# Performance work log

Measured on AMD Instinct MI355X. Metric: run time of the kernel, lower is better.

Reference implementation:

```python
import jax, jax.numpy as jnp
import numpy as np
import math

H, W = 512, 1024
PS = 2
H_p, W_p = H // PS, W // PS
N = 9
C_IN, C_OUT = 128, 64
GROUPS = 32
B = 2
EPS_GN = 1e-5


def _make_grid():
    # Replicates LatDeform2xDown buffers: centers + sec(lat)-scaled 3x3 offsets.
    pr = np.arange(H_p, dtype=np.float32) * PS + (PS - 1) / 2
    pc = np.arange(W_p, dtype=np.float32) * PS + (PS - 1) / 2
    cy = pr / (H - 1) * 2 - 1
    cx = pc / (W - 1) * 2 - 1
    centers = np.stack([np.broadcast_to(cx[None, :], (H_p, W_p)),
                        np.broadcast_to(cy[:, None], (H_p, W_p))], axis=-1)  # (H_p,W_p,2)
    delta = math.pi / (H - 1)  # drop_south_pole = False
    lat = math.pi / 2 - pr * delta
    sec_max = W / 4.0
    sec = np.clip(1.0 / np.cos(lat), -sec_max, sec_max).astype(np.float32)
    ky, kx = np.meshgrid(np.array([-1.0, 0.0, 1.0], np.float32),
                         np.array([-1.0, 0.0, 1.0], np.float32), indexing='ij')
    kxf, kyf = kx.flatten(), ky.flatten()
    dx = (kxf[None, :] * sec[:, None]) / (W - 1) * 2          # (H_p, 9)
    dy = np.broadcast_to(kyf[None, :], (H_p, N)) / (H - 1) * 2  # (H_p, 9)
    offsets = np.stack([dx, dy], axis=-1)                      # (H_p, 9, 2)
    locs = centers[:, :, None, :] + offsets[:, None, :, :]     # (H_p, W_p, 9, 2)
    return jnp.asarray(locs.reshape(-1, 2).astype(np.float32))


def group_norm(x, gamma, beta, groups, eps=EPS_GN):
    b, c, h, w = x.shape
    xg = x.reshape(b, groups, c // groups, h, w)
    mu = xg.mean(axis=(2, 3, 4), keepdims=True)
    var = ((xg - mu) ** 2).mean(axis=(2, 3, 4), keepdims=True)
    xn = ((xg - mu) * jax.lax.rsqrt(var + eps)).reshape(b, c, h, w)
    return xn * gamma[None, :, None, None] + beta[None, :, None, None]


def setup_inputs() -> dict:
    key = jax.random.key(0)
    ks = jax.random.split(key, 3)
    x = jax.random.normal(ks[0], (B, C_IN, H_p, W_p), dtype=jnp.float32)
    w_conv = jax.random.normal(ks[1], (N * C_OUT, C_IN), dtype=jnp.float32) * 0.02
    w_post = jax.random.normal(ks[2], (C_OUT, C_OUT), dtype=jnp.float32) * 0.05
    return {
        'x': x,
        'grid': _make_grid(),
        'gamma1': jnp.ones((C_IN,), jnp.float32),
        'beta1': jnp.zeros((C_IN,), jnp.float32),
        'w_conv': w_conv,
        'splat_bias': jnp.zeros((C_OUT,), jnp.float32),
        'w_post': w_post,
        'b_post': jnp.zeros((C_OUT,), jnp.float32),
        'gamma2': jnp.ones((C_OUT,), jnp.float32),
        'beta2': jnp.zeros((C_OUT,), jnp.float32),
    }


def reference(x, grid, gamma1, beta1, w_conv, splat_bias, w_post, b_post, gamma2, beta2):
    b = x.shape[0]
    # norm + 1x1 conv (no bias): Wx part of the Wx+b split
    h = group_norm(x, gamma1, beta1, GROUPS)
    vals = jnp.einsum('oc,bchw->bohw', w_conv, h)                 # (B, 9*C, H_p, W_p)
    vals = vals.reshape(b, C_OUT, N, H_p, W_p).transpose(0, 1, 3, 4, 2)
    vals = vals.reshape(b, C_OUT, H_p * W_p * N)                  # (B, C, M)

    # bilinear splat coordinates
    px = (grid[:, 0] + 1.0) * 0.5 * (W - 1)                       # (M,)
    py = (grid[:, 1] + 1.0) * 0.5 * (H - 1)
    x0 = jnp.floor(px).astype(jnp.int32)
    y0 = jnp.floor(py).astype(jnp.int32)
    x1, y1 = x0 + 1, y0 + 1
    fx = px - x0.astype(px.dtype)
    fy = py - y0.astype(py.dtype)
    w00 = (1 - fx) * (1 - fy)
    w01 = (1 - fx) * fy
    w10 = fx * (1 - fy)
    w11 = fx * fy
    x0w = x0 % W
    x1w = x1 % W
    half_W = W // 2

    def polar_wrap(yi, xi):
        past_n = yi < 0
        past_s = yi >= H
        yi = jnp.where(past_n, -yi, yi)
        yi = jnp.where(past_s, 2 * H - yi, yi)
        xi = jnp.where(past_n | past_s, (xi + half_W) % W, xi)
        return jnp.clip(yi, 0, H - 1), xi

    num = jnp.zeros((b, C_OUT, H * W), x.dtype)
    den = jnp.zeros((H * W,), x.dtype)  # identical across batch in the original
    for wt, yi, xi in ((w00, y0, x0w), (w01, y1, x0w), (w10, y0, x1w), (w11, y1, x1w)):
        yi, xi = polar_wrap(yi, xi)
        idx = yi * W + xi                                          # (M,)
        num = num.at[:, :, idx].add(vals * wt[None, None, :])
        den = den.at[idx].add(wt)

    out = num / jnp.clip(den, 1e-8)[None, None, :]
    out = out.reshape(b, C_OUT, H, W) + splat_bias[None, :, None, None]
    # post: 1x1 conv + GroupNorm + exact GELU
    out = jnp.einsum('oc,bchw->bohw', w_post, out) + b_post[None, :, None, None]
    out = group_norm(out, gamma2, beta2, GROUPS)
    return jax.nn.gelu(out, approximate=False)
```

## Files before the change

kernel.cpp:

```cpp
#include <hip/hip_runtime.h>
#include <cstdint>
#include <cstddef>

#define H_   512
#define W_   1024
#define HP_  256
#define WP_  512
#define NTAP 9
#define CIN  128
#define COUT 64
#define HWP  (HP_*WP_)
#define MIDX (HWP*NTAP)
#define HW_  (H_*W_)

typedef __attribute__((ext_vector_type(8))) short bhalf8_t;
typedef __attribute__((ext_vector_type(4))) float floatx4_t;

__device__ __forceinline__ unsigned short f2bf(float f) {
    unsigned u = __float_as_uint(f);
    u += 0x7fffu + ((u >> 16) & 1u);
    return (unsigned short)(u >> 16);
}
__device__ __forceinline__ float bf2f(unsigned short s) {
    return __uint_as_float(((unsigned)s) << 16);
}

__global__ __launch_bounds__(256) void k0_prep(
    const float* __restrict__ w_conv, const float* __restrict__ w_post,
    unsigned short* __restrict__ w2, unsigned short* __restrict__ wpostbf,
    float* __restrict__ gnzero ) {
    int idx = blockIdx.x * 256 + threadIdx.x;
    if (idx < 576*128) {
        int r = idx >> 7, c = idx & 127;
        int o = r / 9, n = r % 9;
        w2[((n*64 + o) << 7) + c] = f2bf(w_conv[idx]);
    } else if (idx < 576*128 + 4096) {
        int i2 = idx - 576*128;
        wpostbf[i2] = f2bf(w_post[i2]);
    } else if (idx < 576*128 + 4096 + 256) {
        gnzero[idx - (576*128 + 4096)] = 0.f;
    }
}

__global__ __launch_bounds__(256) void k1_stats(const float* __restrict__ x,
                                                float* __restrict__ gnsum1) {
    __shared__ float red[512];
    int bid = blockIdx.x;
    int b = bid >> 8, rem = bid & 255;
    int g = rem >> 3, slice = rem & 7;
    const float4* xp = (const float4*)x + (size_t)(b*CIN + g*4) * (HWP/4) + (size_t)slice*16384;
    float s = 0.f, s2 = 0.f;
    for (int i = threadIdx.x; i < 16384; i += 256) {
        float4 v = xp[i];
        s  += v.x + v.y + v.z + v.w;
        s2 += v.x*v.x + v.y*v.y + v.z*v.z + v.w*v.w;
    }
    red[threadIdx.x] = s; red[256 + threadIdx.x] = s2;
    __syncthreads();
    for (int off = 128; off > 0; off >>= 1) {
        if (threadIdx.x < off) {
            red[threadIdx.x] += red[threadIdx.x + off];
            red[256 + threadIdx.x] += red[256 + threadIdx.x + off];
        }
        __syncthreads();
    }
    if (threadIdx.x == 0) {
        atomicAdd(&gnsum1[(b*32 + g)*2],     red[0]);
        atomicAdd(&gnsum1[(b*32 + g)*2 + 1], red[256]);
    }
}

__global__ void k1b_coef(const float* __restrict__ gnsum1,
                         const float* __restrict__ gamma1, const float* __restrict__ beta1,
                         float* __restrict__ acoef, float* __restrict__ bcoef) {
    int t = threadIdx.x;
    int b = t >> 7, c = t & 127, g = c >> 2;
    float s1 = gnsum1[(b*32+g)*2], s2 = gnsum1[(b*32+g)*2+1];
    const float inv = 1.f / 524288.f;
    float mean = s1 * inv;
    float var  = s2 * inv - mean*mean;
    float rstd = rsqrtf(var + 1e-5f);
    float a = gamma1[c] * rstd;
    acoef[t] = a;
    bcoef[t] = beta1[c] - mean * a;
}

__global__ __launch_bounds__(256) void k2_conv(
    const float* __restrict__ x, const unsigned short* __restrict__ w2,
    const float* __restrict__ acoef, const float* __restrict__ bcoef,
    unsigned short* __restrict__ vals) {
    __shared__ unsigned short As[64*136];
    __shared__ unsigned short Bs[128*136];
    __shared__ unsigned short Cs[128*72];
    int b   = blockIdx.y;
    int tile = blockIdx.x;
    int pr  = tile >> 2, pcb = (tile & 3) << 7;
    int tid = threadIdx.x;

    for (int task = tid; task < 2048; task += 256) {
        int p = task & 127, c0 = (task >> 7) << 3;
        bhalf8_t t8;
        #pragma unroll
        for (int j = 0; j < 8; ++j) {
            int c = c0 + j;
            float xv = x[(size_t)(b*CIN + c)*HWP + (size_t)pr*WP_ + pcb + p];
            float v = fmaf(xv, acoef[b*CIN + c], bcoef[b*CIN + c]);
            t8[j] = (short)f2bf(v);
        }
        *(bhalf8_t*)&Bs[p*136 + c0] = t8;
    }
    __syncthreads();

    int wave = tid >> 6, lane = tid & 63;
    int l15 = lane & 15, lq = lane >> 4;

    bhalf8_t bfr[2][4];
    #pragma unroll
    for (int ptl = 0; ptl < 2; ++ptl) {
        int p = (wave*2 + ptl)*16 + l15;
        #pragma unroll
        for (int ks = 0; ks < 4; ++ks)
            bfr[ptl][ks] = *(const bhalf8_t*)&Bs[p*136 + ks*32 + lq*8];
    }

    for (int n = 0; n < 9; ++n) {
        __syncthreads();
        for (int i = tid; i < 4096; i += 256) {
            int r = i >> 6, cp = i & 63;
            ((unsigned*)As)[r*68 + cp] = ((const unsigned*)w2)[(n*64 + r)*64 + cp];
        }
        __syncthreads();
        floatx4_t acc[2][4] = {};
        #pragma unroll
        for (int ks = 0; ks < 4; ++ks) {
            bhalf8_t af[4];
            #pragma unroll
            for (int rt = 0; rt < 4; ++rt)
                af[rt] = *(const bhalf8_t*)&As[(rt*16 + l15)*136 + ks*32 + lq*8];
            #pragma unroll
            for (int ptl = 0; ptl < 2; ++ptl)
                #pragma unroll
                for (int rt = 0; rt < 4; ++rt)
                    acc[ptl][rt] = __builtin_amdgcn_mfma_f32_16x16x32_bf16(
                        af[rt], bfr[ptl][ks], acc[ptl][rt], 0, 0, 0);
        }
        #pragma unroll
        for (int ptl = 0; ptl < 2; ++ptl) {
            int p = (wave*2 + ptl)*16 + l15;
            #pragma unroll
            for (int rt = 0; rt < 4; ++rt)
                #pragma unroll
                for (int reg = 0; reg < 4; ++reg) {
                    int o = rt*16 + lq*4 + reg;
                    Cs[p*72 + o] = f2bf(acc[ptl][rt][reg]);
                }
        }
        __syncthreads();
        size_t outbase = (size_t)b*HWP + (size_t)pr*WP_ + pcb;
        for (int i = tid; i < 4096; i += 256) {
            int p = i >> 5, o2 = i & 31;
            ((unsigned*)vals)[((outbase + p)*576 + n*64)/2 + o2] = ((const unsigned*)Cs)[p*36 + o2];
        }
    }
}

__global__ __launch_bounds__(256) void k3_gather(
    const float* __restrict__ gridp, const unsigned short* __restrict__ vals,
    const unsigned short* __restrict__ wpostbf,
    const float* __restrict__ splat_bias, const float* __restrict__ b_post,
    float* __restrict__ out, float* __restrict__ gnsum2) {

    __shared__ unsigned short SM[256*72];
    __shared__ unsigned short WPs[64*72];
    __shared__ float sb_s[64], bp_s[64], gsum[64];

    int tid = threadIdx.x;
    int bx = blockIdx.x;
    int y  = blockIdx.y;
    int b  = blockIdx.z;
    int x  = (bx << 8) + tid;

    if (tid < 64) { sb_s[tid] = splat_bias[tid]; bp_s[tid] = b_post[tid]; gsum[tid] = 0.f; }
    for (int i = tid; i < 2048; i += 256) {
        int r = i >> 5, cp = i & 31;
        ((unsigned*)WPs)[r*36 + cp] = ((const unsigned*)wpostbf)[(r << 5) + cp];
    }

    float num[64];
    #pragma unroll
    for (int c = 0; c < 64; ++c) num[c] = 0.f;
    float den = 0.f;

    const float2* g2 = (const float2*)gridp;
    int prc = y >> 1;
    for (int dpr = -1; dpr <= 1; ++dpr) {
        int pr = prc + dpr;
        if (pr < 0 || pr > HP_-1) continue;
        for (int kyi = 0; kyi < 3; ++kyi) {
            float gy = g2[pr*WP_*9 + kyi*3 + 1].y;
            float py = ((gy + 1.0f) * 0.5f) * 511.0f;
            float y0f = floorf(py);
            float fy = py - y0f;
            int y0i = (int)y0f;
            #pragma unroll
            for (int side = 0; side < 2; ++side) {
                int yi = y0i + side;
                bool pn = yi < 0, ps = yi >= H_;
                int yy = pn ? -yi : (ps ? (2*H_ - yi) : yi);
                yy = min(max(yy, 0), H_-1);
                if (yy != y) continue;
                int sh = (pn || ps) ? (W_/2) : 0;
                float wy = side ? fy : (1.0f - fy);
                for (int kxi = 0; kxi < 3; ++kxi) {
                    int n = kyi*3 + kxi;
                    float gx0 = g2[pr*WP_*9 + n].x;
                    float px0 = ((gx0 + 1.0f) * 0.5f) * 1023.0f;
                    int Tt = x - sh - 1;
                    #pragma unroll
                    for (int j = -1; j <= 1; ++j) {
                        float A = ((float)(Tt + j*W_) - px0) * 0.5f;
                        int clo = (int)ceilf(A - 1e-3f);
                        int chi = (int)floorf(A + 1.001f);
                        for (int pc = clo; pc <= chi; ++pc) {
                            if (pc < 0 || pc >= WP_) continue;
                            int m = (pr*WP_ + pc)*9 + n;
                            float2 g = g2[m];
                            float px = ((g.x + 1.0f) * 0.5f) * 1023.0f;
                            float x0f = floorf(px);
                            float fx = px - x0f;
                            int x0i = (int)x0f;
                            int xl = (x0i + 2*W_ + sh) & (W_-1);
                            float w;
                            if (xl == x)                      w = (1.0f - fx) * wy;
                            else if (((xl + 1) & (W_-1)) == x) w = fx * wy;
                            else continue;
                            den += w;
                            const uint4* vp = (const uint4*)(vals + (((size_t)b*MIDX + m) << 6));
                            #pragma unroll
                            for (int q = 0; q < 8; ++q) {
                                uint4 u = vp[q];
                                unsigned uu[4] = {u.x, u.y, u.z, u.w};
                                #pragma unroll
                                for (int e = 0; e < 4; ++e) {
                                    float lo = __uint_as_float(uu[e] << 16);
                                    float hi = __uint_as_float(uu[e] & 0xffff0000u);
                                    num[q*8 + e*2]     = fmaf(w, lo, num[q*8 + e*2]);
                                    num[q*8 + e*2 + 1] = fmaf(w, hi, num[q*8 + e*2 + 1]);
                                }
                            }
                        }
                    }
                }
            }
        }
    }

    float invd = 1.0f / fmaxf(den, 1e-8f);
    {
        int base = tid * 72;
        #pragma unroll
        for (int c8 = 0; c8 < 8; ++c8) {
            bhalf8_t t8;
            #pragma unroll
            for (int jj = 0; jj < 8; ++jj) {
                float v = fmaf(num[c8*8 + jj], invd, sb_s[c8*8 + jj]);
                t8[jj] = (short)f2bf(v);
            }
            *(bhalf8_t*)&SM[base + c8*8] = t8;
        }
    }
    __syncthreads();

    int wave = tid >> 6, lane = tid & 63, l15 = lane & 15, lq = lane >> 4;
    floatx4_t acc[4][4] = {};
    #pragma unroll
    for (int ks = 0; ks < 2; ++ks) {
        bhalf8_t af[4], bf[4];
        #pragma unroll
        for (int ot = 0; ot < 4; ++ot)
            af[ot] = *(const bhalf8_t*)&WPs[(ot*16 + l15)*72 + ks*32 + lq*8];
        #pragma unroll
        for (int pt = 0; pt < 4; ++pt)
            bf[pt] = *(const bhalf8_t*)&SM[((wave*4 + pt)*16 + l15)*72 + ks*32 + lq*8];
        #pragma unroll
        for (int pt = 0; pt < 4; ++pt)
            #pragma unroll
            for (int ot = 0; ot < 4; ++ot)
                acc[pt][ot] = __builtin_amdgcn_mfma_f32_16x16x32_bf16(
                    af[ot], bf[pt], acc[pt][ot], 0, 0, 0);
    }

    float s1l[8], s2l[8];
    #pragma unroll
    for (int li = 0; li < 8; ++li) { s1l[li] = 0.f; s2l[li] = 0.f; }
    #pragma unroll
    for (int pt = 0; pt < 4; ++pt) {
        int px = (wave*4 + pt)*16 + l15;
        int xg = (bx << 8) + px;
        #pragma unroll
        for (int ot = 0; ot < 4; ++ot)
            #pragma unroll
            for (int reg = 0; reg < 4; ++reg) {
                int o = ot*16 + lq*4 + reg;
                float v = acc[pt][ot][reg] + bp_s[o];
                out[((size_t)(b*64 + o) << 19) + ((size_t)y << 10) + xg] = v;
                int li = ot*2 + (reg >> 1);
                s1l[li] += v;
                s2l[li] += v*v;
            }
    }
    #pragma unroll
    for (int li = 0; li < 8; ++li) {
        int g = (li >> 1)*8 + lq*2 + (li & 1);
        atomicAdd(&gsum[g*2],     s1l[li]);
        atomicAdd(&gsum[g*2 + 1], s2l[li]);
    }
    __syncthreads();
    if (tid < 64) atomicAdd(&gnsum2[b*64 + tid], gsum[tid]);
}

__global__ __launch_bounds__(256) void k5_final(
    float* __restrict__ out, const float* __restrict__ gnsum2,
    const float* __restrict__ gamma2, const float* __restrict__ beta2) {
    size_t idx = (size_t)blockIdx.x * 256 + threadIdx.x;
    size_t e8 = idx << 3;
    int b = (int)(e8 >> 25);
    int o = (int)((e8 >> 19) & 63);
    int g = o >> 1;
    float s1 = gnsum2[b*64 + g*2], s2 = gnsum2[b*64 + g*2 + 1];
    const float invn = 1.0f / 1048576.0f;
    float mean = s1 * invn;
    float var  = s2 * invn - mean*mean;
    float rstd = rsqrtf(var + 1e-5f);
    float sc = gamma2[o] * rstd;
    float sf = beta2[o] - mean * sc;
    float4* p0 = (float4*)(out + e8);
    float4 v0 = p0[0], v1 = p0[1];
    float r[8] = {v0.x, v0.y, v0.z, v0.w, v1.x, v1.y, v1.z, v1.w};
    #pragma unroll
    for (int j = 0; j < 8; ++j) {
        float t = fmaf(r[j], sc, sf);
        r[j] = 0.5f * t * (1.0f + erff(t * 0.70710678118654752f));
    }
    p0[0] = make_float4(r[0], r[1], r[2], r[3]);
    p0[1] = make_float4(r[4], r[5], r[6], r[7]);
}

extern "C" void kernel_launch(void* const* d_in, const int* in_sizes, int n_in,
                              void* d_out, int out_size, void* d_ws, size_t ws_size,
                              hipStream_t stream) {
    const float* x      = (const float*)d_in[0];
    const float* gridp  = (const float*)d_in[1];
    const float* gamma1 = (const float*)d_in[2];
    const float* beta1  = (const float*)d_in[3];
    const float* w_conv = (const float*)d_in[4];
    const float* sbias  = (const float*)d_in[5];
    const float* w_post = (const float*)d_in[6];
    const float* b_post = (const float*)d_in[7];
    const float* gamma2 = (const float*)d_in[8];
    const float* beta2  = (const float*)d_in[9];
    float* out = (float*)d_out;

    char* ws = (char*)d_ws;
    unsigned short* w2      = (unsigned short*)(ws);
    unsigned short* wpostbf = (unsigned short*)(ws + 147456);
    float* gnsum1 = (float*)(ws + 155648);
    float* gnsum2 = (float*)(ws + 156160);
    float* acoef  = (float*)(ws + 156672);
    float* bcoef  = (float*)(ws + 157696);
    unsigned short* vals = (unsigned short*)(ws + 158720);

    hipLaunchKernelGGL(k0_prep,  dim3(305),          dim3(256), 0, stream,
                       w_conv, w_post, w2, wpostbf, gnsum1);
    hipLaunchKernelGGL(k1_stats, dim3(512),          dim3(256), 0, stream, x, gnsum1);
    hipLaunchKernelGGL(k1b_coef, dim3(1),            dim3(256), 0, stream,
                       gnsum1, gamma1, beta1, acoef, bcoef);
    hipLaunchKernelGGL(k2_conv,  dim3(1024, 2),      dim3(256), 0, stream,
                       x, w2, acoef, bcoef, vals);
    hipLaunchKernelGGL(k3_gather, dim3(4, 512, 2),   dim3(256), 0, stream,
                       gridp, vals, wpostbf, sbias, b_post, out, gnsum2);
    hipLaunchKernelGGL(k5_final, dim3(32768),        dim3(256), 0, stream,
                       out, gnsum2, gamma2, beta2);
}
```

Baseline: 994.8 us.

## Fold post 1x1 conv weights into deform conv weights, drop MFMA stage in gather

```diff
diff --git a/kernel.cpp b/kernel.cpp
--- a/kernel.cpp
+++ b/kernel.cpp
@@ -27,18 +27,26 @@
 
 __global__ __launch_bounds__(256) void k0_prep(
     const float* __restrict__ w_conv, const float* __restrict__ w_post,
-    unsigned short* __restrict__ w2, unsigned short* __restrict__ wpostbf,
+    const float* __restrict__ sbias,  const float* __restrict__ b_post,
+    unsigned short* __restrict__ w2, float* __restrict__ sb2,
     float* __restrict__ gnzero ) {
     int idx = blockIdx.x * 256 + threadIdx.x;
-    if (idx < 576*128) {
-        int r = idx >> 7, c = idx & 127;
-        int o = r / 9, n = r % 9;
-        w2[((n*64 + o) << 7) + c] = f2bf(w_conv[idx]);
-    } else if (idx < 576*128 + 4096) {
-        int i2 = idx - 576*128;
-        wpostbf[i2] = f2bf(w_post[i2]);
-    } else if (idx < 576*128 + 4096 + 256) {
-        gnzero[idx - (576*128 + 4096)] = 0.f;
+    if (idx < 73728) {
+        int r = idx >> 7, ci = idx & 127;
+        int n = r >> 6, o = r & 63;
+        float acc = 0.f;
+        #pragma unroll 8
+        for (int op = 0; op < 64; ++op)
+            acc = fmaf(w_post[o*64 + op], w_conv[(op*9 + n)*128 + ci], acc);
+        w2[idx] = f2bf(acc);
+    } else if (idx < 73728 + 64) {
+        int o = idx - 73728;
+        float acc = b_post[o];
+        for (int op = 0; op < 64; ++op)
+            acc = fmaf(w_post[o*64 + op], sbias[op], acc);
+        sb2[o] = acc;
+    } else if (idx < 73728 + 64 + 256) {
+        gnzero[idx - (73728 + 64)] = 0.f;
     }
 }
 
@@ -166,13 +174,11 @@
 
 __global__ __launch_bounds__(256) void k3_gather(
     const float* __restrict__ gridp, const unsigned short* __restrict__ vals,
-    const unsigned short* __restrict__ wpostbf,
-    const float* __restrict__ splat_bias, const float* __restrict__ b_post,
+    const float* __restrict__ sb2g,
     float* __restrict__ out, float* __restrict__ gnsum2) {
 
-    __shared__ unsigned short SM[256*72];
-    __shared__ unsigned short WPs[64*72];
-    __shared__ float sb_s[64], bp_s[64], gsum[64];
+    __shared__ float sb2_s[64];
+    __shared__ float red[256];
 
     int tid = threadIdx.x;
     int bx = blockIdx.x;
@@ -180,11 +186,8 @@
     int b  = blockIdx.z;
     int x  = (bx << 8) + tid;
 
-    if (tid < 64) { sb_s[tid] = splat_bias[tid]; bp_s[tid] = b_post[tid]; gsum[tid] = 0.f; }
-    for (int i = tid; i < 2048; i += 256) {
-        int r = i >> 5, cp = i & 31;
-        ((unsigned*)WPs)[r*36 + cp] = ((const unsigned*)wpostbf)[(r << 5) + cp];
-    }
+    if (tid < 64) sb2_s[tid] = sb2g[tid];
+    __syncthreads();
 
     float num[64];
     #pragma unroll
@@ -256,67 +259,75 @@
     }
 
     float invd = 1.0f / fmaxf(den, 1e-8f);
-    {
-        int base = tid * 72;
-        #pragma unroll
-        for (int c8 = 0; c8 < 8; ++c8) {
-            bhalf8_t t8;
-            #pragma unroll
-            for (int jj = 0; jj < 8; ++jj) {
-                float v = fmaf(num[c8*8 + jj], invd, sb_s[c8*8 + jj]);
-                t8[jj] = (short)f2bf(v);
-            }
-            *(bhalf8_t*)&SM[base + c8*8] = t8;
-        }
-    }
+    size_t obase = ((size_t)b << 25) + ((size_t)y << 10) + (size_t)x;
+    #pragma unroll
+    for (int c = 0; c < 64; ++c) {
+        float v = fmaf(num[c], invd, sb2_s[c]);
+        out[obase + ((size_t)c << 19)] = v;
+        num[c] = v;
+    }
+
+    float st[64];
+    #pragma unroll
+    for (int g = 0; g < 32; ++g) {
+        float a = num[2*g], b2 = num[2*g + 1];
+        st[g]      = a + b2;
+        st[32 + g] = fmaf(a, a, b2*b2);
+    }
+    int lane = tid & 63;
+    float r32[32];
+    { bool hi = (lane & 32) != 0;
+      #pragma unroll
+      for (int j = 0; j < 32; ++j) {
+          float keep = hi ? st[32+j] : st[j];
+          float send = hi ? st[j]    : st[32+j];
+          r32[j] = keep + __shfl_xor(send, 32, 64);
+      } }
+    float r16[16];
+    { bool hi = (lane & 16) != 0;
+      #pragma unroll
+      for (int j = 0; j < 16; ++j) {
+          float keep = hi ? r32[16+j] : r32[j];
+          float send = hi ? r32[j]    : r32[16+j];
+          r16[j] = keep + __shfl_xor(send, 16, 64);
+      } }
+    float r8[8];
+    { bool hi = (lane & 8) != 0;
+      #pragma unroll
+      for (int j = 0; j < 8; ++j) {
+          float keep = hi ? r16[8+j] : r16[j];
+          float send = hi ? r16[j]   : r16[8+j];
+          r8[j] = keep + __shfl_xor(send, 8, 64);
+      } }
+    float r4[4];
+    { bool hi = (lane & 4) != 0;
+      #pragma unroll
+      for (int j = 0; j < 4; ++j) {
+          float keep = hi ? r8[4+j] : r8[j];
+          float send = hi ? r8[j]   : r8[4+j];
+          r4[j] = keep + __shfl_xor(send, 4, 64);
+      } }
+    float r2[2];
+    { bool hi = (lane & 2) != 0;
+      #pragma unroll
+      for (int j = 0; j < 2; ++j) {
+          float keep = hi ? r4[2+j] : r4[j];
+          float send = hi ? r4[j]   : r4[2+j];
+          r2[j] = keep + __shfl_xor(send, 2, 64);
+      } }
+    float r1;
+    { bool hi = (lane & 1) != 0;
+      float keep = hi ? r2[1] : r2[0];
+      float send = hi ? r2[0] : r2[1];
+      r1 = keep + __shfl_xor(send, 1, 64);
+    }
+    red[tid] = r1;
     __syncthreads();
-
-    int wave = tid >> 6, lane = tid & 63, l15 = lane & 15, lq = lane >> 4;
-    floatx4_t acc[4][4] = {};
-    #pragma unroll
-    for (int ks = 0; ks < 2; ++ks) {
-        bhalf8_t af[4], bf[4];
-        #pragma unroll
-        for (int ot = 0; ot < 4; ++ot)
-            af[ot] = *(const bhalf8_t*)&WPs[(ot*16 + l15)*72 + ks*32 + lq*8];
-        #pragma unroll
-        for (int pt = 0; pt < 4; ++pt)
-            bf[pt] = *(const bhalf8_t*)&SM[((wave*4 + pt)*16 + l15)*72 + ks*32 + lq*8];
-        #pragma unroll
-        for (int pt = 0; pt < 4; ++pt)
-            #pragma unroll
-            for (int ot = 0; ot < 4; ++ot)
-                acc[pt][ot] = __builtin_amdgcn_mfma_f32_16x16x32_bf16(
-                    af[ot], bf[pt], acc[pt][ot], 0, 0, 0);
-    }
-
-    float s1l[8], s2l[8];
-    #pragma unroll
-    for (int li = 0; li < 8; ++li) { s1l[li] = 0.f; s2l[li] = 0.f; }
-    #pragma unroll
-    for (int pt = 0; pt < 4; ++pt) {
-        int px = (wave*4 + pt)*16 + l15;
-        int xg = (bx << 8) + px;
-        #pragma unroll
-        for (int ot = 0; ot < 4; ++ot)
-            #pragma unroll
-            for (int reg = 0; reg < 4; ++reg) {
-                int o = ot*16 + lq*4 + reg;
-                float v = acc[pt][ot][reg] + bp_s[o];
-                out[((size_t)(b*64 + o) << 19) + ((size_t)y << 10) + xg] = v;
-                int li = ot*2 + (reg >> 1);
-                s1l[li] += v;
-                s2l[li] += v*v;
-            }
-    }
-    #pragma unroll
-    for (int li = 0; li < 8; ++li) {
-        int g = (li >> 1)*8 + lq*2 + (li & 1);
-        atomicAdd(&gsum[g*2],     s1l[li]);
-        atomicAdd(&gsum[g*2 + 1], s2l[li]);
-    }
-    __syncthreads();
-    if (tid < 64) atomicAdd(&gnsum2[b*64 + tid], gsum[tid]);
+    if (tid < 64) {
+        float tot = red[tid] + red[tid + 64] + red[tid + 128] + red[tid + 192];
+        int slot = (tid < 32) ? (tid << 1) : (((tid - 32) << 1) + 1);
+        atomicAdd(&gnsum2[(b << 6) + slot], tot);
+    }
 }
 
 __global__ __launch_bounds__(256) void k5_final(
@@ -362,23 +373,23 @@
     float* out = (float*)d_out;
 
     char* ws = (char*)d_ws;
-    unsigned short* w2      = (unsigned short*)(ws);
-    unsigned short* wpostbf = (unsigned short*)(ws + 147456);
-    float* gnsum1 = (float*)(ws + 155648);
-    float* gnsum2 = (float*)(ws + 156160);
-    float* acoef  = (float*)(ws + 156672);
-    float* bcoef  = (float*)(ws + 157696);
-    unsigned short* vals = (unsigned short*)(ws + 158720);
-
-    hipLaunchKernelGGL(k0_prep,  dim3(305),          dim3(256), 0, stream,
-                       w_conv, w_post, w2, wpostbf, gnsum1);
+    unsigned short* w2 = (unsigned short*)(ws);
+    float* gnsum1 = (float*)(ws + 147456);
+    float* gnsum2 = (float*)(ws + 147968);
+    float* acoef  = (float*)(ws + 148480);
+    float* bcoef  = (float*)(ws + 149504);
+    float* sb2    = (float*)(ws + 150528);
+    unsigned short* vals = (unsigned short*)(ws + 150784);
+
+    hipLaunchKernelGGL(k0_prep,  dim3(290),          dim3(256), 0, stream,
+                       w_conv, w_post, sbias, b_post, w2, sb2, gnsum1);
     hipLaunchKernelGGL(k1_stats, dim3(512),          dim3(256), 0, stream, x, gnsum1);
     hipLaunchKernelGGL(k1b_coef, dim3(1),            dim3(256), 0, stream,
                        gnsum1, gamma1, beta1, acoef, bcoef);
     hipLaunchKernelGGL(k2_conv,  dim3(1024, 2),      dim3(256), 0, stream,
                        x, w2, acoef, bcoef, vals);
     hipLaunchKernelGGL(k3_gather, dim3(4, 512, 2),   dim3(256), 0, stream,
-                       gridp, vals, wpostbf, sbias, b_post, out, gnsum2);
+                       gridp, vals, sb2, out, gnsum2);
     hipLaunchKernelGGL(k5_final, dim3(32768),        dim3(256), 0, stream,
                        out, gnsum2, gamma2, beta2);
 }
```

Result: faster. 886.7 us (-10.9%).
